# Kernel tuning notes

Measured on AMD Instinct MI355X. Metric: run time of the kernel, lower is better.

Reference implementation:

```python
import jax, jax.numpy as jnp
import numpy as np

N = 10000        # num_nodes
F_IN = 256       # dataset_num_features
H = 128          # hidden_channels
C_OUT = 40       # dataset_num_classes
L = 3            # num_layers
HEADS = 8
DH = H // HEADS  # per-head dim
E = 160000       # num edges (before self loops)
SCALE = 1.0 / float(np.sqrt(DH))


def setup_inputs() -> dict:
    key = jax.random.key(0)
    ks = jax.random.split(key, 8)
    s = lambda k, *sh: (jax.random.normal(k, sh, dtype=jnp.float32) * 0.05)
    return dict(
        edge_index=jax.random.randint(ks[0], (2, E), 0, N, dtype=jnp.int32),
        x_param=s(ks[1], N, F_IN),
        lin1_w=s(ks[2], F_IN, H),
        lin1_b=jnp.zeros((H,), jnp.float32),
        wq=s(ks[3], L, H, H),
        wk=s(ks[4], L, H, H),
        wv=s(ks[5], L, H, H),
        bq=jnp.zeros((L, H), jnp.float32),
        bk=jnp.zeros((L, H), jnp.float32),
        bv=jnp.zeros((L, H), jnp.float32),
        lin2_w=s(ks[6], H, C_OUT),
        lin2_b=jnp.zeros((C_OUT,), jnp.float32),
    )


def _gcn_norm(edge_index):
    # PyG gcn_norm: add self loops (weight 1), symmetric D^-1/2 A D^-1/2
    loops = jnp.arange(N, dtype=edge_index.dtype)
    row = jnp.concatenate([edge_index[0], loops])  # source j
    col = jnp.concatenate([edge_index[1], loops])  # target i
    deg = jax.ops.segment_sum(jnp.ones(row.shape, jnp.float32), col, num_segments=N)
    dis = jnp.where(deg > 0, jax.lax.rsqrt(jnp.maximum(deg, 1e-12)), 0.0)
    return row, col, dis[row] * dis[col]


def _restricted_softmax(score):
    # softmax with an implicit extra logit at `margin=0`
    m = jnp.maximum(jnp.max(score, axis=-1, keepdims=True), 0.0)
    e = jnp.exp(score - m)
    return e / (jnp.sum(e, axis=-1, keepdims=True) + jnp.exp(-m))


def _forward(edge_index, x_param, lin1_w, lin1_b, wq, wk, wv, bq, bk, bv, lin2_w, lin2_b):
    row, col, norm = _gcn_norm(edge_index)
    # dropouts are eval-mode no-ops
    x = jax.nn.relu(x_param @ lin1_w + lin1_b)  # [N, H]
    x_all = x[:, None, :]                       # [N, 1, H]
    for l in range(L):
        t = x_all.shape[1]
        # project per-node first (linear commutes with per-edge gather)
        q = (x_all[:, -1] @ wq[l] + bq[l]).reshape(N, HEADS, DH)      # query from latest state
        k = (x_all @ wk[l] + bk[l]).reshape(N, t, HEADS, DH)          # keys over full history
        v = (x_all @ wv[l] + bv[l]).reshape(N, t, HEADS, DH)
        qe = q[col]   # [Etot, heads, dh]   (x_i)
        ke = k[row]   # [Etot, t, heads, dh] (x_j)
        ve = v[row]
        score = jnp.einsum('ehd,ethd->eht', qe, ke) * SCALE
        attn = _restricted_softmax(score)        # attention-dropout is a no-op in eval
        msg = jnp.einsum('eht,ethd->ehd', attn, ve).reshape(-1, H) * norm[:, None]
        out = jax.ops.segment_sum(msg, col, num_segments=N)  # aggr='add'
        x = jax.nn.relu(out)
        x_all = jnp.concatenate([x_all, x[:, None, :]], axis=1)
    logits = x_all[:, -1] @ lin2_w + lin2_b
    return jax.nn.log_softmax(logits, axis=1)


def reference(edge_index, x_param, lin1_w, lin1_b, wq, wk, wv, bq, bk, bv, lin2_w, lin2_b):
    return _forward(edge_index, x_param, lin1_w, lin1_b, wq, wk, wv, bq, bk, bv, lin2_w, lin2_b)
```

## Files before the change

### kernel.cpp

```cpp
#include <hip/hip_runtime.h>
#include <math.h>

#define N_NODES 10000
#define F_IN_D  256
#define H_DIM   128
#define C_OUTD  40
#define NHEADS  8
#define NEDGES  160000
#define ETOT    (NEDGES + N_NODES)
#define SCALE_F 0.25f
#define TILES_N 157
#define KVSZ    ((size_t)N_NODES * 3 * 256)

typedef __attribute__((ext_vector_type(8))) short bf16x8;
typedef __attribute__((ext_vector_type(4))) float f32x4;
typedef __attribute__((ext_vector_type(2))) float f32x2;

__device__ __forceinline__ unsigned short f2bf(float f) {
    unsigned int u = __float_as_uint(f);
    unsigned int r = (u + 0x7FFFu + ((u >> 16) & 1u)) >> 16;
    return (unsigned short)r;
}
__device__ __forceinline__ float bf2f(unsigned short h) {
    return __uint_as_float(((unsigned int)h) << 16);
}
__device__ __forceinline__ unsigned char f2fp8(float v) {
    int pk = __builtin_amdgcn_cvt_pk_fp8_f32(v, v, 0, false);
    return (unsigned char)(pk & 0xff);
}


__global__ __launch_bounds__(256) void k_prep1(const float* __restrict__ w1,
                                               unsigned short* __restrict__ W1T,
                                               int* __restrict__ degi) {
    int t = blockIdx.x * 256 + threadIdx.x;
    if (t < 8192) {
        float4 v = *(const float4*)(w1 + 4 * t);
        int e = 4 * t;
        #pragma unroll
        for (int i = 0; i < 4; ++i) {
            int k = (e + i) >> 7, n = (e + i) & 127;
            W1T[n * 256 + k] = f2bf(((const float*)&v)[i]);
        }
    } else if (t < 10692) {
        int idx = (t - 8192) * 4;
        *(int4*)&degi[idx] = make_int4(0, 0, 0, 0);
    }
}


__device__ __forceinline__ void lin1_block(int bid, int ct0, const float* __restrict__ X,
                                           const unsigned short* __restrict__ W1T,
                                           const float* __restrict__ b1,
                                           unsigned short* __restrict__ X0, int nct) {
    int tid = threadIdx.x;
    int wid = tid >> 6, lane = tid & 63;
    int m = lane & 15, quad = lane >> 4;
    int rowA = bid * 64 + wid * 16 + m;
    int rowc = rowA < N_NODES ? rowA : N_NODES - 1;
    bf16x8 af[8];
    const float* ap = X + (size_t)rowc * F_IN_D + quad * 8;
    #pragma unroll
    for (int s = 0; s < 8; ++s) {
        float4 lo = *(const float4*)(ap + s * 32);
        float4 hi = *(const float4*)(ap + s * 32 + 4);
        union { unsigned short u[8]; bf16x8 v; } pk;
        pk.u[0] = f2bf(lo.x); pk.u[1] = f2bf(lo.y);
        pk.u[2] = f2bf(lo.z); pk.u[3] = f2bf(lo.w);
        pk.u[4] = f2bf(hi.x); pk.u[5] = f2bf(hi.y);
        pk.u[6] = f2bf(hi.z); pk.u[7] = f2bf(hi.w);
        af[s] = pk.v;
    }
    int row0 = bid * 64 + wid * 16 + quad * 4;
    for (int ct = ct0; ct < ct0 + nct; ++ct) {
        int col = ct * 16 + m;
        const unsigned short* bp = W1T + (size_t)col * F_IN_D + quad * 8;
        f32x4 acc = {0.f, 0.f, 0.f, 0.f};
        #pragma unroll
        for (int s = 0; s < 8; ++s) {
            bf16x8 bfr = __builtin_bit_cast(bf16x8, *(const uint4*)(bp + s * 32));
            acc = __builtin_amdgcn_mfma_f32_16x16x32_bf16(af[s], bfr, acc, 0, 0, 0);
        }
        float bb = b1[col];
        #pragma unroll
        for (int rg = 0; rg < 4; ++rg) {
            int r = row0 + rg;
            if (r < N_NODES)
                X0[(size_t)r * H_DIM + col] = f2bf(fmaxf(acc[rg] + bb, 0.f));
        }
    }
}

__device__ __forceinline__ void qkv_block(int mi, int rt,
                                          const unsigned short* __restrict__ XHb,
                                          const unsigned short* __restrict__ WTq_l,
                                          const unsigned short* __restrict__ WTk_l,
                                          const unsigned short* __restrict__ WTv_l,
                                          const float* __restrict__ bq_l,
                                          const float* __restrict__ bk_l,
                                          const float* __restrict__ bv_l,
                                          unsigned short* __restrict__ Qb,
                                          unsigned char* __restrict__ KVb,
                                          int hasQ, int qslice, int nK, int sbase,
                                          int cp0, int nct) {
    int tid = threadIdx.x;
    int wid = tid >> 6, lane = tid & 63;
    int m = lane & 15, quad = lane >> 4;
    const unsigned short* WT; const float* bias; int slice, mode;
    if (hasQ && mi == 0) { WT = WTq_l; bias = bq_l; slice = qslice; mode = 0; }
    else {
        int j = mi - hasQ;
        if (j < nK) { WT = WTk_l; bias = bk_l; slice = sbase + j;      mode = 1; }
        else        { WT = WTv_l; bias = bv_l; slice = sbase + j - nK; mode = 2; }
    }
    const unsigned short* A = XHb + (size_t)slice * N_NODES * H_DIM;
    int rowA = rt * 64 + wid * 16 + m;
    bf16x8 af[4];
    const unsigned short* ap = A + (size_t)rowA * H_DIM + quad * 8;
    #pragma unroll
    for (int s = 0; s < 4; ++s)
        af[s] = __builtin_bit_cast(bf16x8, *(const uint4*)(ap + s * 32));
    int row0 = rt * 64 + wid * 16 + quad * 4;
    int vofs = (mode == 2) ? 8 : 0;
    for (int cp = cp0; cp < cp0 + nct; ++cp) {
        int colA = cp * 32 + m;
        int colB = colA + 16;
        const unsigned short* bpA = WT + (size_t)colA * H_DIM + quad * 8;
        const unsigned short* bpB = WT + (size_t)colB * H_DIM + quad * 8;
        bf16x8 bA[4], bB[4];
        #pragma unroll
        for (int s = 0; s < 4; ++s) {
            bA[s] = __builtin_bit_cast(bf16x8, *(const uint4*)(bpA + s * 32));
            bB[s] = __builtin_bit_cast(bf16x8, *(const uint4*)(bpB + s * 32));
        }
        f32x4 accA = {0.f, 0.f, 0.f, 0.f};
        f32x4 accB = {0.f, 0.f, 0.f, 0.f};
        #pragma unroll
        for (int s = 0; s < 4; ++s) {
            accA = __builtin_amdgcn_mfma_f32_16x16x32_bf16(af[s], bA[s], accA, 0, 0, 0);
            accB = __builtin_amdgcn_mfma_f32_16x16x32_bf16(af[s], bB[s], accB, 0, 0, 0);
        }
        float bbA = bias[colA], bbB = bias[colB];
        #pragma unroll
        for (int rg = 0; rg < 4; ++rg) {
            int r = row0 + rg;
            if (r < N_NODES) {
                float vA = accA[rg] + bbA;
                float vB = accB[rg] + bbB;
                if (mode == 0) {
                    Qb[(size_t)r * H_DIM + colA] = f2bf(vA * SCALE_F);
                    Qb[(size_t)r * H_DIM + colB] = f2bf(vB * SCALE_F);
                } else {
                    size_t nb = ((size_t)r * 3 + slice) * 256;
                    KVb[nb + (colA >> 3) * 16 + (colA & 7) + vofs] = f2fp8(vA);
                    KVb[nb + (colB >> 3) * 16 + (colB & 7) + vofs] = f2fp8(vB);
                }
            }
        }
    }
}


template <int T>
__device__ __forceinline__ void kv_load(const uint4* __restrict__ KV, int r, int ci,
                                        uint4 (&kv)[T]) {
    const uint4* p = KV + (size_t)r * 48 + ci;
    #pragma unroll
    for (int s = 0; s < T; ++s) kv[s] = p[s * 16];
}

template <int T>
__device__ __forceinline__ void edge_accum(const uint4 (&kv)[T], const float (&q)[8],
                                           float nrm, float (&a)[8]) {
    float den = 1.f;
    float mv[8];
    #pragma unroll
    for (int i = 0; i < 8; ++i) mv[i] = 0.f;
    #pragma unroll
    for (int s = 0; s < T; ++s) {
        f32x2 k0 = __builtin_amdgcn_cvt_pk_f32_fp8(kv[s].x, false);
        f32x2 k1 = __builtin_amdgcn_cvt_pk_f32_fp8(kv[s].x, true);
        f32x2 k2 = __builtin_amdgcn_cvt_pk_f32_fp8(kv[s].y, false);
        f32x2 k3 = __builtin_amdgcn_cvt_pk_f32_fp8(kv[s].y, true);
        float p = q[0] * k0[0] + q[1] * k0[1] + q[2] * k1[0] + q[3] * k1[1]
                + q[4] * k2[0] + q[5] * k2[1] + q[6] * k3[0] + q[7] * k3[1];
        p += __shfl_xor(p, 1, 2);
        float w = __expf(p);
        den += w;
        f32x2 v0 = __builtin_amdgcn_cvt_pk_f32_fp8(kv[s].z, false);
        f32x2 v1 = __builtin_amdgcn_cvt_pk_f32_fp8(kv[s].z, true);
        f32x2 v2 = __builtin_amdgcn_cvt_pk_f32_fp8(kv[s].w, false);
        f32x2 v3 = __builtin_amdgcn_cvt_pk_f32_fp8(kv[s].w, true);
        mv[0] += w * v0[0]; mv[1] += w * v0[1];
        mv[2] += w * v1[0]; mv[3] += w * v1[1];
        mv[4] += w * v2[0]; mv[5] += w * v2[1];
        mv[6] += w * v3[0]; mv[7] += w * v3[1];
    }
    float ws = __fdividef(nrm, den);
    #pragma unroll
    for (int i = 0; i < 8; ++i) a[i] += ws * mv[i];
}

template <int T, bool LOGITS>
__device__ __forceinline__ void attn_block(int bid, const unsigned short* __restrict__ Q,
                                           const uint4* __restrict__ KV,
                                           const int2* __restrict__ csr,
                                           const int* __restrict__ degi,
                                           unsigned int* __restrict__ Xout,
                                           const unsigned short* __restrict__ W2T,
                                           const float* __restrict__ b2,
                                           float* __restrict__ out) {
    int tid = threadIdx.x;
    int wid = tid >> 6, lane = tid & 63;
    int quarter = lane >> 4, ci = lane & 15;
    int n = bid * 4 + wid;

    int cnt = degi[n] + 1;
    if (cnt > 64) cnt = 64;
    int li = lane < cnt ? lane : cnt - 1;
    int2 eAll = csr[(n << 6) + li];
    int   rAll = eAll.x;
    float nAll = (lane < cnt) ? __int_as_float(eAll.y) : 0.f;

    float q[8];
    {
        uint4 qp = *(const uint4*)&Q[(size_t)n * H_DIM + ci * 8];
        q[0] = __uint_as_float(qp.x << 16);
        q[1] = __uint_as_float(qp.x & 0xffff0000u);
        q[2] = __uint_as_float(qp.y << 16);
        q[3] = __uint_as_float(qp.y & 0xffff0000u);
        q[4] = __uint_as_float(qp.z << 16);
        q[5] = __uint_as_float(qp.z & 0xffff0000u);
        q[6] = __uint_as_float(qp.w << 16);
        q[7] = __uint_as_float(qp.w & 0xffff0000u);
    }
    int nq = (cnt + 3) >> 2;
    float a[8];
    #pragma unroll
    for (int i = 0; i < 8; ++i) a[i] = 0.f;

    auto rowN = [&](int j4) { return __shfl(rAll, j4 < 63 ? j4 : 63, 64); };
    auto nrmN = [&](int j4) { return __shfl(nAll, j4 < 63 ? j4 : 63, 64); };

    uint4 kv0[T], kv1[T], kv2[T], kv3[T];
    kv_load<T>(KV, rowN(quarter), ci, kv0);
    kv_load<T>(KV, rowN(4 + quarter), ci, kv1);
    kv_load<T>(KV, rowN(8 + quarter), ci, kv2);
    kv_load<T>(KV, rowN(12 + quarter), ci, kv3);

    int j = 0;
    for (;;) {
        edge_accum<T>(kv0, q, nrmN(j * 4 + quarter), a);
        if (++j >= nq) break;
        kv_load<T>(KV, rowN((j + 3) * 4 + quarter), ci, kv0);
        edge_accum<T>(kv1, q, nrmN(j * 4 + quarter), a);
        if (++j >= nq) break;
        kv_load<T>(KV, rowN((j + 3) * 4 + quarter), ci, kv1);
        edge_accum<T>(kv2, q, nrmN(j * 4 + quarter), a);
        if (++j >= nq) break;
        kv_load<T>(KV, rowN((j + 3) * 4 + quarter), ci, kv2);
        edge_accum<T>(kv3, q, nrmN(j * 4 + quarter), a);
        if (++j >= nq) break;
        kv_load<T>(KV, rowN((j + 3) * 4 + quarter), ci, kv3);
    }

    #pragma unroll
    for (int i = 0; i < 8; ++i) {
        a[i] += __shfl_xor(a[i], 16, 64);
        a[i] += __shfl_xor(a[i], 32, 64);
    }

    if (!LOGITS) {
        if (quarter == 0) {
            uint4 o;
            o.x = ((unsigned int)f2bf(fmaxf(a[1], 0.f)) << 16) | (unsigned int)f2bf(fmaxf(a[0], 0.f));
            o.y = ((unsigned int)f2bf(fmaxf(a[3], 0.f)) << 16) | (unsigned int)f2bf(fmaxf(a[2], 0.f));
            o.z = ((unsigned int)f2bf(fmaxf(a[5], 0.f)) << 16) | (unsigned int)f2bf(fmaxf(a[4], 0.f));
            o.w = ((unsigned int)f2bf(fmaxf(a[7], 0.f)) << 16) | (unsigned int)f2bf(fmaxf(a[6], 0.f));
            *(uint4*)&Xout[(size_t)n * 64 + ci * 4] = o;
        }
        return;
    }

    float x[8];
    #pragma unroll
    for (int i = 0; i < 8; ++i) x[i] = fmaxf(a[i], 0.f);
    float lg[10];
    #pragma unroll
    for (int jj = 0; jj < 10; ++jj) {
        int c = quarter * 10 + jj;
        uint4 w = *(const uint4*)&W2T[c * H_DIM + ci * 8];
        float p = x[0] * bf2f((unsigned short)(w.x & 0xffff))
                + x[1] * bf2f((unsigned short)(w.x >> 16))
                + x[2] * bf2f((unsigned short)(w.y & 0xffff))
                + x[3] * bf2f((unsigned short)(w.y >> 16))
                + x[4] * bf2f((unsigned short)(w.z & 0xffff))
                + x[5] * bf2f((unsigned short)(w.z >> 16))
                + x[6] * bf2f((unsigned short)(w.w & 0xffff))
                + x[7] * bf2f((unsigned short)(w.w >> 16));
        #pragma unroll
        for (int o = 1; o < 16; o <<= 1) p += __shfl_xor(p, o, 16);
        lg[jj] = p + b2[c];
    }
    float mx = lg[0];
    #pragma unroll
    for (int jj = 1; jj < 10; ++jj) mx = fmaxf(mx, lg[jj]);
    mx = fmaxf(mx, __shfl_xor(mx, 16, 64));
    mx = fmaxf(mx, __shfl_xor(mx, 32, 64));
    float sm = 0.f;
    #pragma unroll
    for (int jj = 0; jj < 10; ++jj) sm += __expf(lg[jj] - mx);
    sm += __shfl_xor(sm, 16, 64);
    sm += __shfl_xor(sm, 32, 64);
    float lse = mx + __logf(sm);
    if (ci == 0) {
        float* op = out + (size_t)n * C_OUTD + quarter * 10;
        #pragma unroll
        for (int jj = 0; jj < 10; ++jj) op[jj] = lg[jj] - lse;
    }
}


__global__ __launch_bounds__(256) void k_deg_lin1(const int* __restrict__ col,
                                                  int* __restrict__ degi,
                                                  int* __restrict__ slotbuf,
                                                  const float* __restrict__ X,
                                                  const unsigned short* __restrict__ W1T,
                                                  const float* __restrict__ b1,
                                                  unsigned short* __restrict__ X0,
                                                  const float* __restrict__ wq,
                                                  const float* __restrict__ wk,
                                                  const float* __restrict__ wv,
                                                  const float* __restrict__ w2,
                                                  unsigned short* __restrict__ WTq,
                                                  unsigned short* __restrict__ WTk,
                                                  unsigned short* __restrict__ WTv,
                                                  unsigned short* __restrict__ W2T,
                                                  int nct) {
    int b = blockIdx.x;
    if (b < 625) {
        int e = b * 256 + threadIdx.x;
        slotbuf[e] = atomicAdd(&degi[col[e]], 1);
        return;
    }
    if (b < 939) {
        int bid = b - 625;
        lin1_block(bid % TILES_N, (bid / TILES_N) * 4, X, W1T, b1, X0, nct);
        return;
    }
    int t = (b - 939) * 256 + threadIdx.x;
    if (t < 36864) {
        int mat = t >> 12;
        int l = mat / 3, ws = mat % 3;
        const float*    src = (ws == 0) ? wq  : (ws == 1) ? wk  : wv;
        unsigned short* dst = (ws == 0) ? WTq : (ws == 1) ? WTk : WTv;
        int e2 = (t & 4095) * 4;
        float4 v = *(const float4*)(src + l * 16384 + e2);
        #pragma unroll
        for (int i = 0; i < 4; ++i) {
            int k = (e2 + i) >> 7, n = (e2 + i) & 127;
            dst[l * 16384 + n * 128 + k] = f2bf(((const float*)&v)[i]);
        }
    } else if (t < 38144) {
        int e = (t - 36864) * 4;
        float4 v = *(const float4*)(w2 + e);
        #pragma unroll
        for (int i = 0; i < 4; ++i) {
            int ee = e + i;
            int k = ee / 40, c = ee - k * 40;
            W2T[c * H_DIM + k] = f2bf(((const float*)&v)[i]);
        }
    }
}

__global__ __launch_bounds__(256) void k_scatter_qkv0(const int* __restrict__ row,
                                                      const int* __restrict__ col,
                                                      const int* __restrict__ degi,
                                                      const int* __restrict__ slotbuf,
                                                      int2* __restrict__ csr,
                                                      const unsigned short* __restrict__ XHb,
                                                      const unsigned short* __restrict__ WTq,
                                                      const unsigned short* __restrict__ WTk,
                                                      const unsigned short* __restrict__ WTv,
                                                      const float* __restrict__ bq,
                                                      const float* __restrict__ bk,
                                                      const float* __restrict__ bv,
                                                      unsigned short* __restrict__ Qb,
                                                      unsigned char* __restrict__ KVb) {
    if (blockIdx.x < 665) {
        int e = blockIdx.x * 256 + threadIdx.x;
        if (e >= ETOT) return;
        int r, c, slot;
        if (e < NEDGES) { r = row[e]; c = col[e]; slot = slotbuf[e]; }
        else            { r = c = e - NEDGES; slot = degi[c]; }
        if (slot > 63) slot = 63;
        float dr = rsqrtf((float)(degi[r] + 1));
        float dc = rsqrtf((float)(degi[c] + 1));
        int2 ent; ent.x = r; ent.y = __float_as_int(dr * dc);
        csr[(c << 6) + slot] = ent;
        return;
    }
    int b = blockIdx.x - 665;
    int half = b / (3 * TILES_N);
    int bb = b % (3 * TILES_N);
    qkv_block(bb / TILES_N, bb % TILES_N, XHb, WTq, WTk, WTv, bq, bk, bv,
              Qb, KVb, 1, 0, 1, 0, half * 2, 2);
}

template <int T>
__global__ __launch_bounds__(256) void k_attn_qkvold(const unsigned short* __restrict__ Q,
                                                     const uint4* __restrict__ KV,
                                                     const int2* __restrict__ csr,
                                                     const int* __restrict__ degi,
                                                     unsigned int* __restrict__ Xout,
                                                     const unsigned short* __restrict__ XHb,
                                                     const unsigned short* __restrict__ WTk_l,
                                                     const unsigned short* __restrict__ WTv_l,
                                                     const float* __restrict__ bk_l,
                                                     const float* __restrict__ bv_l,
                                                     unsigned char* __restrict__ KVnext,
                                                     int nK) {
    if (blockIdx.x < 2500) {
        attn_block<T, false>(blockIdx.x, Q, KV, csr, degi, Xout,
                             nullptr, nullptr, nullptr);
        return;
    }
    int b = blockIdx.x - 2500;
    qkv_block(b / TILES_N, b % TILES_N, XHb, nullptr, WTk_l, WTv_l,
              nullptr, bk_l, bv_l, nullptr, KVnext, 0, 0, nK, 0, 0, 4);
}

__global__ __launch_bounds__(256) void k_qkv(const unsigned short* __restrict__ XHb,
                                             const unsigned short* __restrict__ WTq_l,
                                             const unsigned short* __restrict__ WTk_l,
                                             const unsigned short* __restrict__ WTv_l,
                                             const float* __restrict__ bq_l,
                                             const float* __restrict__ bk_l,
                                             const float* __restrict__ bv_l,
                                             unsigned short* __restrict__ Qb,
                                             unsigned char* __restrict__ KVb,
                                             int qslice) {
    int half = blockIdx.x / (3 * TILES_N);
    int bb = blockIdx.x % (3 * TILES_N);
    qkv_block(bb / TILES_N, bb % TILES_N, XHb, WTq_l, WTk_l, WTv_l,
              bq_l, bk_l, bv_l, Qb, KVb, 1, qslice, 1, qslice, half * 2, 2);
}

__global__ __launch_bounds__(256) void k_attn_logits(const unsigned short* __restrict__ Q,
                                                     const uint4* __restrict__ KV,
                                                     const int2* __restrict__ csr,
                                                     const int* __restrict__ degi,
                                                     const unsigned short* __restrict__ W2T,
                                                     const float* __restrict__ b2,
                                                     float* __restrict__ out) {
    attn_block<3, true>(blockIdx.x, Q, KV, csr, degi, nullptr, W2T, b2, out);
}


extern "C" void kernel_launch(void* const* d_in, const int* in_sizes, int n_in,
                              void* d_out, int out_size, void* d_ws, size_t ws_size,
                              hipStream_t stream) {
    const int*   ei      = (const int*)d_in[0];
    const int*   row     = ei;
    const int*   col     = ei + NEDGES;
    const float* x_param = (const float*)d_in[1];
    const float* lin1_w  = (const float*)d_in[2];
    const float* lin1_b  = (const float*)d_in[3];
    const float* wq      = (const float*)d_in[4];
    const float* wk      = (const float*)d_in[5];
    const float* wv      = (const float*)d_in[6];
    const float* bq      = (const float*)d_in[7];
    const float* bk      = (const float*)d_in[8];
    const float* bv      = (const float*)d_in[9];
    const float* lin2_w  = (const float*)d_in[10];
    const float* lin2_b  = (const float*)d_in[11];
    float*       out     = (float*)d_out;

    char* wbase = (char*)d_ws;
    size_t off = 0;
    auto alloc = [&](size_t bytes) -> void* {
        off = (off + 255) & ~(size_t)255;
        void* p = wbase + off;
        off += bytes;
        return p;
    };
    int*            degi     = (int*)           alloc((size_t)N_NODES * 4);
    int*            slotbuf  = (int*)           alloc((size_t)NEDGES * 4);
    int2*           csr      = (int2*)          alloc((size_t)N_NODES * 64 * 8);
    unsigned short* W1T      = (unsigned short*)alloc((size_t)H_DIM * F_IN_D * 2);
    unsigned short* WTq      = (unsigned short*)alloc((size_t)3 * H_DIM * H_DIM * 2);
    unsigned short* WTk      = (unsigned short*)alloc((size_t)3 * H_DIM * H_DIM * 2);
    unsigned short* WTv      = (unsigned short*)alloc((size_t)3 * H_DIM * H_DIM * 2);
    unsigned short* W2T      = (unsigned short*)alloc((size_t)C_OUTD * H_DIM * 2);
    unsigned short* XHb      = (unsigned short*)alloc((size_t)3 * N_NODES * H_DIM * 2);
    unsigned short* Qb       = (unsigned short*)alloc((size_t)N_NODES * H_DIM * 2);
    unsigned char*  KVb      = (unsigned char*) alloc(2 * KVSZ);

    k_prep1<<<42, 256, 0, stream>>>(lin1_w, W1T, degi);

    k_deg_lin1<<<1089, 256, 0, stream>>>(col, degi, slotbuf,
                                         x_param, W1T, lin1_b, XHb,
                                         wq, wk, wv, lin2_w,
                                         WTq, WTk, WTv, W2T, 4);

    k_scatter_qkv0<<<665 + 6 * TILES_N, 256, 0, stream>>>(
        row, col, degi, slotbuf, csr,
        XHb, WTq, WTk, WTv, bq, bk, bv, Qb, KVb);

    unsigned int* X1 = (unsigned int*)(XHb + (size_t)1 * N_NODES * H_DIM);
    unsigned int* X2 = (unsigned int*)(XHb + (size_t)2 * N_NODES * H_DIM);

    k_attn_qkvold<1><<<2500 + 2 * TILES_N, 256, 0, stream>>>(
        Qb, (const uint4*)KVb, csr, degi, X1,
        XHb, WTk + 16384, WTv + 16384, bk + H_DIM, bv + H_DIM,
        KVb + KVSZ, 1);

    k_qkv<<<6 * TILES_N, 256, 0, stream>>>(
        XHb, WTq + 16384, WTk + 16384, WTv + 16384,
        bq + H_DIM, bk + H_DIM, bv + H_DIM, Qb, KVb + KVSZ, 1);

    k_attn_qkvold<2><<<2500 + 4 * TILES_N, 256, 0, stream>>>(
        Qb, (const uint4*)(KVb + KVSZ), csr, degi, X2,
        XHb, WTk + 2 * 16384, WTv + 2 * 16384, bk + 2 * H_DIM, bv + 2 * H_DIM,
        KVb, 2);

    k_qkv<<<6 * TILES_N, 256, 0, stream>>>(
        XHb, WTq + 2 * 16384, WTk + 2 * 16384, WTv + 2 * 16384,
        bq + 2 * H_DIM, bk + 2 * H_DIM, bv + 2 * H_DIM, Qb, KVb, 2);

    k_attn_logits<<<2500, 256, 0, stream>>>(Qb, (const uint4*)KVb, csr, degi,
                                            W2T, lin2_b, out);
}
```

Measured before the change: 217.1 us.

## Triple-buffer KV history and regroup QKV projections across layer launches

Replaces the two-buffer KV ping-pong with three per-layer KV buffers, so projections of older history states for later layers can be computed earlier and grouped into shared launches. The attention kernel for layer 0 also projects layer-1 and layer-2 keys and values of the input features. A combined kernel computes the layer-1 projections of the newest state together with the layer-2 projections of the previous state, so layer 2's attention runs as a pure kernel. QKV blocks now split work into quarters instead of halves, giving more, smaller blocks. The cost is a larger workspace and a reshuffled dependency schedule.

```diff
diff --git a/kernel.cpp b/kernel.cpp
--- a/kernel.cpp
+++ b/kernel.cpp
@@ -401,49 +401,95 @@
         return;
     }
     int b = blockIdx.x - 665;
-    int half = b / (3 * TILES_N);
+    int quarter = b / (3 * TILES_N);
     int bb = b % (3 * TILES_N);
     qkv_block(bb / TILES_N, bb % TILES_N, XHb, WTq, WTk, WTv, bq, bk, bv,
-              Qb, KVb, 1, 0, 1, 0, half * 2, 2);
-}
-
-template <int T>
-__global__ __launch_bounds__(256) void k_attn_qkvold(const unsigned short* __restrict__ Q,
-                                                     const uint4* __restrict__ KV,
-                                                     const int2* __restrict__ csr,
-                                                     const int* __restrict__ degi,
-                                                     unsigned int* __restrict__ Xout,
-                                                     const unsigned short* __restrict__ XHb,
-                                                     const unsigned short* __restrict__ WTk_l,
-                                                     const unsigned short* __restrict__ WTv_l,
-                                                     const float* __restrict__ bk_l,
-                                                     const float* __restrict__ bv_l,
-                                                     unsigned char* __restrict__ KVnext,
-                                                     int nK) {
+              Qb, KVb, 1, 0, 1, 0, quarter, 1);
+}
+
+__global__ __launch_bounds__(256) void k_attn0_old(const unsigned short* __restrict__ Q,
+                                                   const uint4* __restrict__ KV,
+                                                   const int2* __restrict__ csr,
+                                                   const int* __restrict__ degi,
+                                                   unsigned int* __restrict__ Xout,
+                                                   const unsigned short* __restrict__ XHb,
+                                                   const unsigned short* __restrict__ WTk,
+                                                   const unsigned short* __restrict__ WTv,
+                                                   const float* __restrict__ bk,
+                                                   const float* __restrict__ bv,
+                                                   unsigned char* __restrict__ B1,
+                                                   unsigned char* __restrict__ B2) {
     if (blockIdx.x < 2500) {
-        attn_block<T, false>(blockIdx.x, Q, KV, csr, degi, Xout,
+        attn_block<1, false>(blockIdx.x, Q, KV, csr, degi, Xout,
                              nullptr, nullptr, nullptr);
         return;
     }
-    int b = blockIdx.x - 2500;
-    qkv_block(b / TILES_N, b % TILES_N, XHb, nullptr, WTk_l, WTv_l,
-              nullptr, bk_l, bv_l, nullptr, KVnext, 0, 0, nK, 0, 0, 4);
-}
-
-__global__ __launch_bounds__(256) void k_qkv(const unsigned short* __restrict__ XHb,
-                                             const unsigned short* __restrict__ WTq_l,
-                                             const unsigned short* __restrict__ WTk_l,
-                                             const unsigned short* __restrict__ WTv_l,
-                                             const float* __restrict__ bq_l,
-                                             const float* __restrict__ bk_l,
-                                             const float* __restrict__ bv_l,
-                                             unsigned short* __restrict__ Qb,
-                                             unsigned char* __restrict__ KVb,
-                                             int qslice) {
-    int half = blockIdx.x / (3 * TILES_N);
+    int bb = blockIdx.x - 2500;
+    int layer = bb / (2 * TILES_N);
+    int r = bb % (2 * TILES_N);
+    int mi = r / TILES_N;
+    int rt = r % TILES_N;
+    int woff = (layer + 1) * 16384;
+    unsigned char* dst = layer ? B2 : B1;
+    qkv_block(mi, rt, XHb, nullptr, WTk + woff, WTv + woff, nullptr,
+              bk + (layer + 1) * H_DIM, bv + (layer + 1) * H_DIM, nullptr,
+              dst, 0, 0, 1, 0, 0, 4);
+}
+
+__global__ __launch_bounds__(256) void k_qkvnew1_old2b(const unsigned short* __restrict__ XHb,
+                                                       const unsigned short* __restrict__ WTq,
+                                                       const unsigned short* __restrict__ WTk,
+                                                       const unsigned short* __restrict__ WTv,
+                                                       const float* __restrict__ bq,
+                                                       const float* __restrict__ bk,
+                                                       const float* __restrict__ bv,
+                                                       unsigned short* __restrict__ Qb,
+                                                       unsigned char* __restrict__ B1,
+                                                       unsigned char* __restrict__ B2) {
+    int b = blockIdx.x;
+    if (b < 12 * TILES_N) {
+        int quarter = b / (3 * TILES_N);
+        int bb = b % (3 * TILES_N);
+        qkv_block(bb / TILES_N, bb % TILES_N, XHb,
+                  WTq + 16384, WTk + 16384, WTv + 16384,
+                  bq + H_DIM, bk + H_DIM, bv + H_DIM,
+                  Qb, B1, 1, 1, 1, 1, quarter, 1);
+        return;
+    }
+    int b2 = b - 12 * TILES_N;
+    int quarter = b2 / (2 * TILES_N);
+    int bb = b2 % (2 * TILES_N);
+    int mi = bb / TILES_N;
+    qkv_block(mi, bb % TILES_N, XHb, nullptr, WTk + 32768, WTv + 32768, nullptr,
+              bk + 2 * H_DIM, bv + 2 * H_DIM, nullptr,
+              B2, 0, 0, 1, 1, quarter, 1);
+}
+
+template <int T>
+__global__ __launch_bounds__(256) void k_attn_pure(const unsigned short* __restrict__ Q,
+                                                   const uint4* __restrict__ KV,
+                                                   const int2* __restrict__ csr,
+                                                   const int* __restrict__ degi,
+                                                   unsigned int* __restrict__ Xout) {
+    attn_block<T, false>(blockIdx.x, Q, KV, csr, degi, Xout,
+                         nullptr, nullptr, nullptr);
+}
+
+__global__ __launch_bounds__(256) void k_qkv2(const unsigned short* __restrict__ XHb,
+                                              const unsigned short* __restrict__ WTq,
+                                              const unsigned short* __restrict__ WTk,
+                                              const unsigned short* __restrict__ WTv,
+                                              const float* __restrict__ bq,
+                                              const float* __restrict__ bk,
+                                              const float* __restrict__ bv,
+                                              unsigned short* __restrict__ Qb,
+                                              unsigned char* __restrict__ B2) {
+    int quarter = blockIdx.x / (3 * TILES_N);
     int bb = blockIdx.x % (3 * TILES_N);
-    qkv_block(bb / TILES_N, bb % TILES_N, XHb, WTq_l, WTk_l, WTv_l,
-              bq_l, bk_l, bv_l, Qb, KVb, 1, qslice, 1, qslice, half * 2, 2);
+    qkv_block(bb / TILES_N, bb % TILES_N, XHb,
+              WTq + 32768, WTk + 32768, WTv + 32768,
+              bq + 2 * H_DIM, bk + 2 * H_DIM, bv + 2 * H_DIM,
+              Qb, B2, 1, 2, 1, 2, quarter, 1);
 }
 
 __global__ __launch_bounds__(256) void k_attn_logits(const unsigned short* __restrict__ Q,
@@ -494,7 +540,10 @@
     unsigned short* W2T      = (unsigned short*)alloc((size_t)C_OUTD * H_DIM * 2);
     unsigned short* XHb      = (unsigned short*)alloc((size_t)3 * N_NODES * H_DIM * 2);
     unsigned short* Qb       = (unsigned short*)alloc((size_t)N_NODES * H_DIM * 2);
-    unsigned char*  KVb      = (unsigned char*) alloc(2 * KVSZ);
+    unsigned char*  KVb      = (unsigned char*) alloc(3 * KVSZ);
+    unsigned char*  B0 = KVb;
+    unsigned char*  B1 = KVb + KVSZ;
+    unsigned char*  B2 = KVb + 2 * KVSZ;
 
     k_prep1<<<42, 256, 0, stream>>>(lin1_w, W1T, degi);
 
@@ -503,31 +552,25 @@
                                          wq, wk, wv, lin2_w,
                                          WTq, WTk, WTv, W2T, 4);
 
-    k_scatter_qkv0<<<665 + 6 * TILES_N, 256, 0, stream>>>(
+    k_scatter_qkv0<<<665 + 12 * TILES_N, 256, 0, stream>>>(
         row, col, degi, slotbuf, csr,
-        XHb, WTq, WTk, WTv, bq, bk, bv, Qb, KVb);
+        XHb, WTq, WTk, WTv, bq, bk, bv, Qb, B0);
 
     unsigned int* X1 = (unsigned int*)(XHb + (size_t)1 * N_NODES * H_DIM);
     unsigned int* X2 = (unsigned int*)(XHb + (size_t)2 * N_NODES * H_DIM);
 
-    k_attn_qkvold<1><<<2500 + 2 * TILES_N, 256, 0, stream>>>(
-        Qb, (const uint4*)KVb, csr, degi, X1,
-        XHb, WTk + 16384, WTv + 16384, bk + H_DIM, bv + H_DIM,
-        KVb + KVSZ, 1);
-
-    k_qkv<<<6 * TILES_N, 256, 0, stream>>>(
-        XHb, WTq + 16384, WTk + 16384, WTv + 16384,
-        bq + H_DIM, bk + H_DIM, bv + H_DIM, Qb, KVb + KVSZ, 1);
-
-    k_attn_qkvold<2><<<2500 + 4 * TILES_N, 256, 0, stream>>>(
-        Qb, (const uint4*)(KVb + KVSZ), csr, degi, X2,
-        XHb, WTk + 2 * 16384, WTv + 2 * 16384, bk + 2 * H_DIM, bv + 2 * H_DIM,
-        KVb, 2);
-
-    k_qkv<<<6 * TILES_N, 256, 0, stream>>>(
-        XHb, WTq + 2 * 16384, WTk + 2 * 16384, WTv + 2 * 16384,
-        bq + 2 * H_DIM, bk + 2 * H_DIM, bv + 2 * H_DIM, Qb, KVb, 2);
-
-    k_attn_logits<<<2500, 256, 0, stream>>>(Qb, (const uint4*)KVb, csr, degi,
+    k_attn0_old<<<2500 + 4 * TILES_N, 256, 0, stream>>>(
+        Qb, (const uint4*)B0, csr, degi, X1,
+        XHb, WTk, WTv, bk, bv, B1, B2);
+
+    k_qkvnew1_old2b<<<20 * TILES_N, 256, 0, stream>>>(
+        XHb, WTq, WTk, WTv, bq, bk, bv, Qb, B1, B2);
+
+    k_attn_pure<2><<<2500, 256, 0, stream>>>(Qb, (const uint4*)B1, csr, degi, X2);
+
+    k_qkv2<<<12 * TILES_N, 256, 0, stream>>>(
+        XHb, WTq, WTk, WTv, bq, bk, bv, Qb, B2);
+
+    k_attn_logits<<<2500, 256, 0, stream>>>(Qb, (const uint4*)B2, csr, degi,
                                             W2T, lin2_b, out);
 }
```

Result: no change. 219.3 us (+1.0%).

## Build CSR directly in degree pass and compute edge norms on the fly

Applied to the files above, without the earlier changes.

The degree-counting atomic pass now writes the source node straight into the per-target CSR slot, which removes the separate slot buffer and the scatter kernel. The CSR shrinks from (row, norm) pairs to row ids only. The attention kernels rebuild the symmetric normalisation from degrees with rsqrt, which adds an extra gather of degi[r] per edge. The self loop is now implied at the last valid lane, and the layer-0 QKV projection runs as its own k_qkv launch.

```diff
diff --git a/kernel.cpp b/kernel.cpp
--- a/kernel.cpp
+++ b/kernel.cpp
@@ -7,7 +7,6 @@
 #define C_OUTD  40
 #define NHEADS  8
 #define NEDGES  160000
-#define ETOT    (NEDGES + N_NODES)
 #define SCALE_F 0.25f
 #define TILES_N 157
 #define KVSZ    ((size_t)N_NODES * 3 * 256)
@@ -204,7 +203,7 @@
 template <int T, bool LOGITS>
 __device__ __forceinline__ void attn_block(int bid, const unsigned short* __restrict__ Q,
                                            const uint4* __restrict__ KV,
-                                           const int2* __restrict__ csr,
+                                           const int* __restrict__ csr,
                                            const int* __restrict__ degi,
                                            unsigned int* __restrict__ Xout,
                                            const unsigned short* __restrict__ W2T,
@@ -215,12 +214,15 @@
     int quarter = lane >> 4, ci = lane & 15;
     int n = bid * 4 + wid;
 
-    int cnt = degi[n] + 1;
+    int dn = degi[n];
+    int cnt = dn + 1;
     if (cnt > 64) cnt = 64;
-    int li = lane < cnt ? lane : cnt - 1;
-    int2 eAll = csr[(n << 6) + li];
-    int   rAll = eAll.x;
-    float nAll = (lane < cnt) ? __int_as_float(eAll.y) : 0.f;
+    float rn = rsqrtf((float)(dn + 1));
+    int csrv = csr[(n << 6) + lane];
+    int r = (lane < cnt - 1) ? csrv : n;
+    int dr = degi[r];
+    int   rAll = r;
+    float nAll = (lane < cnt) ? rsqrtf((float)(dr + 1)) * rn : 0.f;
 
     float q[8];
     {
@@ -321,26 +323,29 @@
 }
 
 
-__global__ __launch_bounds__(256) void k_deg_lin1(const int* __restrict__ col,
-                                                  int* __restrict__ degi,
-                                                  int* __restrict__ slotbuf,
-                                                  const float* __restrict__ X,
-                                                  const unsigned short* __restrict__ W1T,
-                                                  const float* __restrict__ b1,
-                                                  unsigned short* __restrict__ X0,
-                                                  const float* __restrict__ wq,
-                                                  const float* __restrict__ wk,
-                                                  const float* __restrict__ wv,
-                                                  const float* __restrict__ w2,
-                                                  unsigned short* __restrict__ WTq,
-                                                  unsigned short* __restrict__ WTk,
-                                                  unsigned short* __restrict__ WTv,
-                                                  unsigned short* __restrict__ W2T,
-                                                  int nct) {
+__global__ __launch_bounds__(256) void k_degsc_lin1(const int* __restrict__ erow,
+                                                    const int* __restrict__ ecol,
+                                                    int* __restrict__ degi,
+                                                    int* __restrict__ csr,
+                                                    const float* __restrict__ X,
+                                                    const unsigned short* __restrict__ W1T,
+                                                    const float* __restrict__ b1,
+                                                    unsigned short* __restrict__ X0,
+                                                    const float* __restrict__ wq,
+                                                    const float* __restrict__ wk,
+                                                    const float* __restrict__ wv,
+                                                    const float* __restrict__ w2,
+                                                    unsigned short* __restrict__ WTq,
+                                                    unsigned short* __restrict__ WTk,
+                                                    unsigned short* __restrict__ WTv,
+                                                    unsigned short* __restrict__ W2T,
+                                                    int nct) {
     int b = blockIdx.x;
     if (b < 625) {
         int e = b * 256 + threadIdx.x;
-        slotbuf[e] = atomicAdd(&degi[col[e]], 1);
+        int c = ecol[e];
+        int slot = atomicAdd(&degi[c], 1);
+        if (slot < 64) csr[(c << 6) + slot] = erow[e];
         return;
     }
     if (b < 939) {
@@ -371,63 +376,6 @@
             W2T[c * H_DIM + k] = f2bf(((const float*)&v)[i]);
         }
     }
-}
-
-__global__ __launch_bounds__(256) void k_scatter_qkv0(const int* __restrict__ row,
-                                                      const int* __restrict__ col,
-                                                      const int* __restrict__ degi,
-                                                      const int* __restrict__ slotbuf,
-                                                      int2* __restrict__ csr,
-                                                      const unsigned short* __restrict__ XHb,
-                                                      const unsigned short* __restrict__ WTq,
-                                                      const unsigned short* __restrict__ WTk,
-                                                      const unsigned short* __restrict__ WTv,
-                                                      const float* __restrict__ bq,
-                                                      const float* __restrict__ bk,
-                                                      const float* __restrict__ bv,
-                                                      unsigned short* __restrict__ Qb,
-                                                      unsigned char* __restrict__ KVb) {
-    if (blockIdx.x < 665) {
-        int e = blockIdx.x * 256 + threadIdx.x;
-        if (e >= ETOT) return;
-        int r, c, slot;
-        if (e < NEDGES) { r = row[e]; c = col[e]; slot = slotbuf[e]; }
-        else            { r = c = e - NEDGES; slot = degi[c]; }
-        if (slot > 63) slot = 63;
-        float dr = rsqrtf((float)(degi[r] + 1));
-        float dc = rsqrtf((float)(degi[c] + 1));
-        int2 ent; ent.x = r; ent.y = __float_as_int(dr * dc);
-        csr[(c << 6) + slot] = ent;
-        return;
-    }
-    int b = blockIdx.x - 665;
-    int half = b / (3 * TILES_N);
-    int bb = b % (3 * TILES_N);
-    qkv_block(bb / TILES_N, bb % TILES_N, XHb, WTq, WTk, WTv, bq, bk, bv,
-              Qb, KVb, 1, 0, 1, 0, half * 2, 2);
-}
-
-template <int T>
-__global__ __launch_bounds__(256) void k_attn_qkvold(const unsigned short* __restrict__ Q,
-                                                     const uint4* __restrict__ KV,
-                                                     const int2* __restrict__ csr,
-                                                     const int* __restrict__ degi,
-                                                     unsigned int* __restrict__ Xout,
-                                                     const unsigned short* __restrict__ XHb,
-                                                     const unsigned short* __restrict__ WTk_l,
-                                                     const unsigned short* __restrict__ WTv_l,
-                                                     const float* __restrict__ bk_l,
-                                                     const float* __restrict__ bv_l,
-                                                     unsigned char* __restrict__ KVnext,
-                                                     int nK) {
-    if (blockIdx.x < 2500) {
-        attn_block<T, false>(blockIdx.x, Q, KV, csr, degi, Xout,
-                             nullptr, nullptr, nullptr);
-        return;
-    }
-    int b = blockIdx.x - 2500;
-    qkv_block(b / TILES_N, b % TILES_N, XHb, nullptr, WTk_l, WTv_l,
-              nullptr, bk_l, bv_l, nullptr, KVnext, 0, 0, nK, 0, 0, 4);
 }
 
 __global__ __launch_bounds__(256) void k_qkv(const unsigned short* __restrict__ XHb,
@@ -446,9 +394,32 @@
               bq_l, bk_l, bv_l, Qb, KVb, 1, qslice, 1, qslice, half * 2, 2);
 }
 
+template <int T>
+__global__ __launch_bounds__(256) void k_attn_qkvold(const unsigned short* __restrict__ Q,
+                                                     const uint4* __restrict__ KV,
+                                                     const int* __restrict__ csr,
+                                                     const int* __restrict__ degi,
+                                                     unsigned int* __restrict__ Xout,
+                                                     const unsigned short* __restrict__ XHb,
+                                                     const unsigned short* __restrict__ WTk_l,
+                                                     const unsigned short* __restrict__ WTv_l,
+                                                     const float* __restrict__ bk_l,
+                                                     const float* __restrict__ bv_l,
+                                                     unsigned char* __restrict__ KVnext,
+                                                     int nK) {
+    if (blockIdx.x < 2500) {
+        attn_block<T, false>(blockIdx.x, Q, KV, csr, degi, Xout,
+                             nullptr, nullptr, nullptr);
+        return;
+    }
+    int b = blockIdx.x - 2500;
+    qkv_block(b / TILES_N, b % TILES_N, XHb, nullptr, WTk_l, WTv_l,
+              nullptr, bk_l, bv_l, nullptr, KVnext, 0, 0, nK, 0, 0, 4);
+}
+
 __global__ __launch_bounds__(256) void k_attn_logits(const unsigned short* __restrict__ Q,
                                                      const uint4* __restrict__ KV,
-                                                     const int2* __restrict__ csr,
+                                                     const int* __restrict__ csr,
                                                      const int* __restrict__ degi,
                                                      const unsigned short* __restrict__ W2T,
                                                      const float* __restrict__ b2,
@@ -485,8 +456,7 @@
         return p;
     };
     int*            degi     = (int*)           alloc((size_t)N_NODES * 4);
-    int*            slotbuf  = (int*)           alloc((size_t)NEDGES * 4);
-    int2*           csr      = (int2*)          alloc((size_t)N_NODES * 64 * 8);
+    int*            csr      = (int*)           alloc((size_t)N_NODES * 64 * 4);
     unsigned short* W1T      = (unsigned short*)alloc((size_t)H_DIM * F_IN_D * 2);
     unsigned short* WTq      = (unsigned short*)alloc((size_t)3 * H_DIM * H_DIM * 2);
     unsigned short* WTk      = (unsigned short*)alloc((size_t)3 * H_DIM * H_DIM * 2);
@@ -498,14 +468,13 @@
 
     k_prep1<<<42, 256, 0, stream>>>(lin1_w, W1T, degi);
 
-    k_deg_lin1<<<1089, 256, 0, stream>>>(col, degi, slotbuf,
-                                         x_param, W1T, lin1_b, XHb,
-                                         wq, wk, wv, lin2_w,
-                                         WTq, WTk, WTv, W2T, 4);
-
-    k_scatter_qkv0<<<665 + 6 * TILES_N, 256, 0, stream>>>(
-        row, col, degi, slotbuf, csr,
-        XHb, WTq, WTk, WTv, bq, bk, bv, Qb, KVb);
+    k_degsc_lin1<<<1089, 256, 0, stream>>>(row, col, degi, csr,
+                                           x_param, W1T, lin1_b, XHb,
+                                           wq, wk, wv, lin2_w,
+                                           WTq, WTk, WTv, W2T, 4);
+
+    k_qkv<<<6 * TILES_N, 256, 0, stream>>>(
+        XHb, WTq, WTk, WTv, bq, bk, bv, Qb, KVb, 0);
 
     unsigned int* X1 = (unsigned int*)(XHb + (size_t)1 * N_NODES * H_DIM);
     unsigned int* X2 = (unsigned int*)(XHb + (size_t)2 * N_NODES * H_DIM);
```

New measurement: 214.6 us. About the same (-1.1%).
